# Optimization experiments

Measured on AMD Instinct MI355X. Metric: run time of the kernel, lower is better.

The kernel has to match this reference:

```python
import jax, jax.numpy as jnp
import numpy as np

B, T, M, P = 512, 64, 256, 256


def setup_inputs() -> dict:
    key = jax.random.key(0)
    ks = jax.random.split(key, 17)
    w = lambda i, shape: (jax.random.normal(ks[i], shape, jnp.float32) * 0.05)
    return {
        "encoded_inputs": jax.random.normal(ks[0], (B, T, M), jnp.float32),
        "y": jax.random.normal(ks[1], (B, T, 1), jnp.float32),
        "tar": jax.random.normal(ks[2], (B, 2), jnp.float32),
        "train": 1,
        "Wd_w": w(3, (M, 2 * P)), "Wd_b": w(4, (M,)),
        "Ud_w": w(5, (M, M)),
        "vd_w": w(6, (1, M)),
        "wt_w": w(7, (1, M + 1)), "wt_b": w(8, (1,)),
        "Wy_w": w(9, (P, P + M)), "Wy_b": w(10, (P,)),
        "vy_w": w(11, (1, P)), "vy_b": w(12, (1,)),
        "Wih": w(13, (4 * P, 1)), "Whh": w(14, (4 * P, P)),
        "bih": w(15, (4 * P,)), "bhh": w(16, (4 * P,)),
    }


def _lstm_cell(x, h, c, Wih, Whh, bih, bhh):
    # torch.nn.LSTMCell gate order: i, f, g, o
    g = x @ Wih.T + h @ Whh.T + (bih + bhh)
    i, f, gg, o = jnp.split(g, 4, axis=1)
    c = jax.nn.sigmoid(f) * c + jax.nn.sigmoid(i) * jnp.tanh(gg)
    h = jax.nn.sigmoid(o) * jnp.tanh(c)
    return h, c


def reference(encoded_inputs, y, tar, train,
              Wd_w, Wd_b, Ud_w, vd_w, wt_w, wt_b,
              Wy_w, Wy_b, vy_w, vy_b, Wih, Whh, bih, bhh):
    Bn = encoded_inputs.shape[0]
    Pn = Whh.shape[1]
    Mn = encoded_inputs.shape[2]
    h0 = jnp.zeros((Bn, Pn), encoded_inputs.dtype)
    c0 = jnp.zeros((Bn, Pn), encoded_inputs.dtype)
    ctx0 = jnp.zeros((Bn, Mn), encoded_inputs.dtype)
    # U_d(encoded_inputs) is loop-invariant
    y1 = jnp.einsum('btm,nm->btn', encoded_inputs, Ud_w)  # (B,T,M)

    def attend(h, s):
        x1 = jnp.concatenate([h, s], axis=1) @ Wd_w.T + Wd_b      # (B,M)
        z1 = jnp.tanh(x1[:, None, :] + y1)                        # (B,T,M)
        l = jnp.einsum('btm,m->bt', z1, vd_w[0])                  # (B,T)
        beta = jax.nn.softmax(l, axis=1)
        return jnp.einsum('bt,btm->bm', beta, encoded_inputs)     # (B,M)

    def step(carry, y_t):
        h, s, _ = carry
        c_t = attend(h, s)
        y_til = jnp.concatenate([c_t, y_t], axis=1) @ wt_w.T + wt_b  # (B,1)
        h, s = _lstm_cell(y_til, h, s, Wih, Whh, bih, bhh)
        return (h, s, c_t), None

    (h, s, c_t), _ = jax.lax.scan(step, (h0, c0, ctx0), jnp.swapaxes(y, 0, 1))

    def head(h):
        return (jnp.concatenate([h, c_t], axis=1) @ Wy_w.T + Wy_b) @ vy_w.T + vy_b

    def extra(h, s, inp):
        y_til = jnp.concatenate([c_t, inp], axis=1) @ wt_w.T + wt_b
        h, s = _lstm_cell(y_til, h, s, Wih, Whh, bih, bhh)
        return h, s, head(h)

    y_Tp1 = head(h)
    if train:
        h, s, y_Tp2 = extra(h, s, tar[:, 0:1])
        h, s, y_Tp3 = extra(h, s, tar[:, 1:2])
    else:
        h, s, y_Tp2 = extra(h, s, y_Tp1)
        h, s, y_Tp3 = extra(h, s, y_Tp2)
    return (y_Tp1, y_Tp2, y_Tp3)
```

## Files before the change

### kernel.cpp

```cpp
#include <hip/hip_runtime.h>


typedef unsigned short u16;
typedef unsigned int u32;
typedef _Float16 half_t;
typedef half_t h2 __attribute__((ext_vector_type(2)));

#define BB 512
#define TT 64
#define MM 256
#define YS 264
#define ES 68
#define NROW 2
#define NTH 1024

#define WD16_OFF  0
#define WHH16_OFF 131072
#define WY16_OFF  393216
#define WQ_ELEMS  524288
#define WQ_BYTES  (WQ_ELEMS * 2)

struct H8 { h2 p[4]; };

#if defined(__has_builtin)
#if __has_builtin(__builtin_amdgcn_fdot2)
#define FDOT2(a, b, c) __builtin_amdgcn_fdot2((a), (b), (c), false)
#endif
#endif
#ifndef FDOT2
__device__ __forceinline__ float FDOT2(h2 a, h2 b, float c) {
  return c + (float)a[0] * (float)b[0] + (float)a[1] * (float)b[1];
}
#endif

__device__ __forceinline__ float dot8(const H8 w, const H8 a, float acc) {
  acc = FDOT2(w.p[0], a.p[0], acc);
  acc = FDOT2(w.p[1], a.p[1], acc);
  acc = FDOT2(w.p[2], a.p[2], acc);
  acc = FDOT2(w.p[3], a.p[3], acc);
  return acc;
}
__device__ __forceinline__ u16 f2h(float f) {
  union { half_t h; u16 u; } x; x.h = (half_t)f; return x.u;
}
__device__ __forceinline__ float h2f(u16 u) {
  union { u16 u; half_t h; } x; x.u = u; return (float)x.h;
}
__device__ __forceinline__ u32 pack2h(float a, float b) {
  union { h2 h; u32 u; } x;
  x.h[0] = (half_t)a; x.h[1] = (half_t)b;
  return x.u;
}
__device__ __forceinline__ h2 u2h2(u32 u) {
  union { u32 u; h2 h; } x; x.u = u; return x.h;
}
__device__ __forceinline__ void unpackH8(const H8 v, float f[8]) {
#pragma unroll
  for (int i = 0; i < 8; ++i) f[i] = (float)v.p[i >> 1][i & 1];
}
__device__ __forceinline__ void ldf8(const float* p, float f[8]) {
  float4 a = *(const float4*)p;
  float4 b = *(const float4*)(p + 4);
  f[0]=a.x; f[1]=a.y; f[2]=a.z; f[3]=a.w;
  f[4]=b.x; f[5]=b.y; f[6]=b.z; f[7]=b.w;
}
__device__ __forceinline__ float tanh_fast(float x) {
  float e = __builtin_amdgcn_exp2f(x * 2.885390081777927f);
  return 1.0f - 2.0f * __builtin_amdgcn_rcpf(1.0f + e);
}
__device__ __forceinline__ float sigmoid_fast(float x) {
  float e = __builtin_amdgcn_exp2f(x * -1.4426950408889634f);
  return __builtin_amdgcn_rcpf(1.0f + e);
}

__global__ __launch_bounds__(256) void prep_kernel(
    const float* __restrict__ Wd, const float* __restrict__ Whh,
    const float* __restrict__ Wy, u16* __restrict__ o) {
  int i = blockIdx.x * 256 + threadIdx.x;
  float v;
  if (i < WHH16_OFF) {
    int ki = i & 7, n = (i >> 3) & 255, kb = i >> 11;
    v = Wd[n * 512 + kb * 8 + ki];
  } else if (i < WY16_OFF) {
    int r = i - WHH16_OFF;
    int ki = r & 7, n = (r >> 3) & 1023, kb = r >> 13;
    v = Whh[n * 256 + kb * 8 + ki];
  } else {
    int r = i - WY16_OFF;
    int ki = r & 7, n = (r >> 3) & 255, kb = r >> 11;
    v = Wy[n * 512 + kb * 8 + ki];
  }
  o[i] = f2h(v);
}

template <int WQ>
__global__ __launch_bounds__(NTH, 4) void scan_kernel(
    const float* __restrict__ E,
    const float* __restrict__ yin,
    const float* __restrict__ tar,
    const int*   __restrict__ train,
    const void*  __restrict__ Wd_q,
    const float* __restrict__ Wd_b,
    const float* __restrict__ Ud_w,
    const float* __restrict__ vd_w,
    const float* __restrict__ wt_w,
    const float* __restrict__ wt_b,
    const void*  __restrict__ Wy_q,
    const float* __restrict__ Wy_b,
    const float* __restrict__ vy_w,
    const float* __restrict__ vy_b,
    const float* __restrict__ Wih,
    const void*  __restrict__ Whh_q,
    const float* __restrict__ bih,
    const float* __restrict__ bhh,
    float* __restrict__ out)
{
  __shared__ __align__(16) u16   y1l[NROW][TT * YS];
  __shared__ __align__(16) u16   e16T[NROW][MM * ES];
  __shared__ __align__(16) u32   hs16[NROW][256];
  __shared__ __align__(16) u32   ctx16p[NROW][128];
  __shared__ __align__(16) float px1[8][MM];
  __shared__ __align__(16) u32   pgs32[8][MM];
  __shared__ __align__(16) float lpart[NROW][4][TT];
  __shared__ __align__(16) u16   betas16[8][TT];
  __shared__ __align__(16) float ysh[NROW][TT];
  __shared__ __align__(16) float ewl[NROW][TT];
  __shared__ float red[16];
  __shared__ float sc[NROW];

  const int j   = threadIdx.x;
  const int n   = j & 255;
  const int grp = j >> 8;
  const int wv  = j >> 6;
  const int b0  = blockIdx.x * NROW;

  if (j < 512) ((u32*)hs16)[j] = 0;
  float creg0 = 0.f, creg1 = 0.f;

  const float wih0 = Wih[n],       wih1 = Wih[n + 256];
  const float wih2 = Wih[n + 512], wih3 = Wih[n + 768];
  const float bb0 = bih[n]       + bhh[n];
  const float bb1 = bih[n + 256] + bhh[n + 256];
  const float bb2 = bih[n + 512] + bhh[n + 512];
  const float bb3 = bih[n + 768] + bhh[n + 768];
  const float wtM = wt_w[MM], wtb = wt_b[0];

  if (j < NROW * TT) {
    const int r = j >> 6, t = j & 63;
    ysh[r][t] = yin[(size_t)(b0 + r) * TT + t];
    const float* __restrict__ Er = E + ((size_t)(b0 + r) * TT + t) * MM;
    float acc = 0.f;
    for (int m0 = 0; m0 < MM; m0 += 8) {
      float e[8], w[8];
      ldf8(Er + m0, e); ldf8(wt_w + m0, w);
#pragma unroll
      for (int m = 0; m < 8; ++m) acc = fmaf(e[m], w[m], acc);
    }
    ewl[r][t] = acc;
  }

  {
    const float* __restrict__ Eb0 = E + (size_t)b0 * TT * MM;
    for (int i = j; i < NROW * TT * MM; i += NTH) {
      int r = i >> 14;
      int idx = i & 16383;
      int t = idx >> 8, m = idx & 255;
      e16T[r][m * ES + t] = f2h(Eb0[i]);
    }
  }

  {
    const int rs = grp >> 1, ths = grp & 1;
    const float* __restrict__ Eb = E + (size_t)(b0 + rs) * TT * MM;
    const float* __restrict__ Uj = Ud_w + (size_t)n * MM;
    for (int t0 = ths * 32; t0 < ths * 32 + 32; t0 += 16) {
      float acc[16];
#pragma unroll
      for (int i = 0; i < 16; ++i) acc[i] = 0.f;
      for (int m0 = 0; m0 < MM; m0 += 8) {
        float w[8]; ldf8(Uj + m0, w);
#pragma unroll
        for (int tt = 0; tt < 16; ++tt) {
          float e[8]; ldf8(Eb + (size_t)(t0 + tt) * MM + m0, e);
#pragma unroll
          for (int mm = 0; mm < 8; ++mm) acc[tt] = fmaf(e[mm], w[mm], acc[tt]);
        }
      }
#pragma unroll
      for (int tt = 0; tt < 16; ++tt)
        y1l[rs][(t0 + tt) * YS + n] = f2h(acc[tt]);
    }
  }
  __syncthreads();

  auto gates_apply = [&](int r, float gi, float gf, float gg, float go,
                         float ytil) {
    gi += ytil * wih0 + bb0;
    gf += ytil * wih1 + bb1;
    gg += ytil * wih2 + bb2;
    go += ytil * wih3 + bb3;
    float& cr = r ? creg1 : creg0;
    float c = sigmoid_fast(gf) * cr + sigmoid_fast(gi) * tanh_fast(gg);
    float h = sigmoid_fast(go) * tanh_fast(c);
    cr = c;
    u16* hsu = (u16*)hs16[r];
    hsu[n] = f2h(h);
    hsu[256 + n] = f2h(c);
  };

  auto whh_gates = [&]() {
    if (wv >= 8) {
      const int jj = j - 512;
      const int n2 = jj & 255, half = jj >> 8;
      float a00 = 0, a01 = 0, a10 = 0, a11 = 0;
      float a20 = 0, a21 = 0, a30 = 0, a31 = 0;
      if (WQ) {
        const u16* __restrict__ base =
            (const u16*)Whh_q + ((size_t)(half * 16) * 1024 + n2) * 8;
#pragma unroll 2
        for (int i = 0; i < 16; ++i) {
          const u16* p = base + (size_t)i * 8192;
          H8 w0 = *(const H8*)p;
          H8 w1 = *(const H8*)(p + 2048);
          H8 w2 = *(const H8*)(p + 4096);
          H8 w3 = *(const H8*)(p + 6144);
          const int kb = half * 16 + i;
          H8 h0v = *(const H8*)&hs16[0][kb * 4];
          H8 h1v = *(const H8*)&hs16[1][kb * 4];
          a00 = dot8(w0, h0v, a00); a01 = dot8(w0, h1v, a01);
          a10 = dot8(w1, h0v, a10); a11 = dot8(w1, h1v, a11);
          a20 = dot8(w2, h0v, a20); a21 = dot8(w2, h1v, a21);
          a30 = dot8(w3, h0v, a30); a31 = dot8(w3, h1v, a31);
        }
      } else {
        const float* __restrict__ base =
            (const float*)Whh_q + (size_t)n2 * 256 + half * 128;
#pragma unroll 2
        for (int i = 0; i < 16; ++i) {
          const int kb = half * 16 + i;
          H8 h0v = *(const H8*)&hs16[0][kb * 4];
          H8 h1v = *(const H8*)&hs16[1][kb * 4];
          float hf0[8], hf1[8]; unpackH8(h0v, hf0); unpackH8(h1v, hf1);
          float w0[8], w1[8], w2[8], w3[8];
          ldf8(base + i * 8, w0);
          ldf8(base + 256 * 256 + i * 8, w1);
          ldf8(base + 512 * 256 + i * 8, w2);
          ldf8(base + 768 * 256 + i * 8, w3);
#pragma unroll
          for (int m = 0; m < 8; ++m) {
            a00 = fmaf(hf0[m], w0[m], a00); a01 = fmaf(hf1[m], w0[m], a01);
            a10 = fmaf(hf0[m], w1[m], a10); a11 = fmaf(hf1[m], w1[m], a11);
            a20 = fmaf(hf0[m], w2[m], a20); a21 = fmaf(hf1[m], w2[m], a21);
            a30 = fmaf(hf0[m], w3[m], a30); a31 = fmaf(hf1[m], w3[m], a31);
          }
        }
      }
      pgs32[(0 << 1) | half][n2] = pack2h(a00, a01);
      pgs32[(1 << 1) | half][n2] = pack2h(a10, a11);
      pgs32[(2 << 1) | half][n2] = pack2h(a20, a21);
      pgs32[(3 << 1) | half][n2] = pack2h(a30, a31);
    }
  };

  auto gates_combine_apply = [&](float yt0, float yt1) {
    h2 i0 = u2h2(pgs32[0][n]), i1 = u2h2(pgs32[1][n]);
    h2 f0 = u2h2(pgs32[2][n]), f1 = u2h2(pgs32[3][n]);
    h2 g0 = u2h2(pgs32[4][n]), g1 = u2h2(pgs32[5][n]);
    h2 o0 = u2h2(pgs32[6][n]), o1 = u2h2(pgs32[7][n]);
    gates_apply(0, (float)i0[0] + (float)i1[0], (float)f0[0] + (float)f1[0],
                (float)g0[0] + (float)g1[0], (float)o0[0] + (float)o1[0], yt0);
    gates_apply(1, (float)i0[1] + (float)i1[1], (float)f0[1] + (float)f1[1],
                (float)g0[1] + (float)g1[1], (float)o0[1] + (float)o1[1], yt1);
  };

  auto head_store = [&](int outIdx) {
    float p = 0.f;
    const int rr = grp >> 1, seg = grp & 1;
    const u32* st = seg ? ctx16p[rr] : hs16[rr];
    if (WQ) {
      const u16* pw = (const u16*)Wy_q + ((size_t)(seg * 32) * 256 + n) * 8;
#pragma unroll 2
      for (int kb = 0; kb < 32; ++kb) {
        H8 w = *(const H8*)pw; pw += 2048;
        H8 s = *(const H8*)&st[kb * 4];
        p = dot8(w, s, p);
      }
    } else {
      const float* W = (const float*)Wy_q + (size_t)n * 512 + seg * 256;
#pragma unroll 2
      for (int kb = 0; kb < 32; ++kb) {
        H8 sv = *(const H8*)&st[kb * 4];
        float sf[8]; unpackH8(sv, sf);
        float w[8]; ldf8(W + kb * 8, w);
#pragma unroll
        for (int i = 0; i < 8; ++i) p = fmaf(sf[i], w[i], p);
      }
    }
    if (grp) px1[grp - 1][n] = p;
    __syncthreads();
    if (grp == 0) {
      float q0 = (p + px1[0][n] + Wy_b[n]) * vy_w[n];
      float q1 = (px1[1][n] + px1[2][n] + Wy_b[n]) * vy_w[n];
#pragma unroll
      for (int off = 32; off; off >>= 1) {
        q0 += __shfl_xor(q0, off, 64);
        q1 += __shfl_xor(q1, off, 64);
      }
      if ((j & 63) == 0) { red[wv] = q0; red[4 + wv] = q1; }
    }
    __syncthreads();
    if (j == 0) {
      float o0 = red[0] + red[1] + red[2] + red[3] + vy_b[0];
      float o1 = red[4] + red[5] + red[6] + red[7] + vy_b[0];
      out[(size_t)outIdx * BB + b0] = o0;
      out[(size_t)outIdx * BB + b0 + 1] = o1;
      sc[0] = o0; sc[1] = o1;
    }
    __syncthreads();
  };

  for (int step = 0; step < TT; ++step) {
    {
      float ax0 = 0.f, ax1 = 0.f;
      if (WQ) {
        const u16* pd = (const u16*)Wd_q + ((size_t)(grp * 16) * 256 + n) * 8;
#pragma unroll 4
        for (int i = 0; i < 16; ++i) {
          H8 w = *(const H8*)pd; pd += 2048;
          const int kb = grp * 16 + i;
          H8 s0 = *(const H8*)&hs16[0][kb * 4];
          H8 s1 = *(const H8*)&hs16[1][kb * 4];
          ax0 = dot8(w, s0, ax0);
          ax1 = dot8(w, s1, ax1);
        }
      } else {
        const float* pd = (const float*)Wd_q + (size_t)n * 512 + grp * 128;
#pragma unroll 2
        for (int i = 0; i < 16; ++i) {
          const int kb = grp * 16 + i;
          H8 s0v = *(const H8*)&hs16[0][kb * 4];
          H8 s1v = *(const H8*)&hs16[1][kb * 4];
          float f0[8], f1[8]; unpackH8(s0v, f0); unpackH8(s1v, f1);
          float w[8]; ldf8(pd + i * 8, w);
#pragma unroll
          for (int m = 0; m < 8; ++m) {
            ax0 = fmaf(f0[m], w[m], ax0);
            ax1 = fmaf(f1[m], w[m], ax1);
          }
        }
      }
      if (grp == 0) { float b = Wd_b[n]; ax0 += b; ax1 += b; }
      px1[grp][n] = ax0;
      px1[4 + grp][n] = ax1;
    }
    __syncthreads();

    if (wv < 8) {
      const int r = j >> 8, e4 = (j >> 6) & 3, t = j & 63;
      const int mb = e4 * 64;
      const u16* __restrict__ yrow = &y1l[r][t * YS + mb];
      const float* __restrict__ p0 = &px1[(r << 2) | 0][mb];
      const float* __restrict__ p1 = &px1[(r << 2) | 1][mb];
      const float* __restrict__ p2 = &px1[(r << 2) | 2][mb];
      const float* __restrict__ p3 = &px1[(r << 2) | 3][mb];
      const float* __restrict__ vp = vd_w + mb;
      float lp = 0.f;
#pragma unroll 2
      for (int m0 = 0; m0 < 64; m0 += 8) {
        float xa[8], xb[8], xc[8], xd[8], vf[8], yf[8];
        ldf8(p0 + m0, xa); ldf8(p1 + m0, xb);
        ldf8(p2 + m0, xc); ldf8(p3 + m0, xd);
        H8 yv = *(const H8*)(yrow + m0); unpackH8(yv, yf);
        ldf8(vp + m0, vf);
#pragma unroll
        for (int mm = 0; mm < 8; ++mm) {
          float z = tanh_fast(xa[mm] + xb[mm] + xc[mm] + xd[mm] + yf[mm]);
          lp = fmaf(z, vf[mm], lp);
        }
      }
      lpart[r][e4][t] = lp;
    } else {
      whh_gates();
    }
    __syncthreads();

    if (j < 256) {
      const int t = j & 63;
      float l0 = lpart[0][0][t] + lpart[0][1][t] + lpart[0][2][t] +
                 lpart[0][3][t];
      float l1 = lpart[1][0][t] + lpart[1][1][t] + lpart[1][2][t] +
                 lpart[1][3][t];
      float m0v = l0, m1v = l1;
#pragma unroll
      for (int off = 32; off; off >>= 1) {
        m0v = fmaxf(m0v, __shfl_xor(m0v, off, 64));
        m1v = fmaxf(m1v, __shfl_xor(m1v, off, 64));
      }
      float e0 = __builtin_amdgcn_exp2f((l0 - m0v) * 1.4426950408889634f);
      float e1 = __builtin_amdgcn_exp2f((l1 - m1v) * 1.4426950408889634f);
      float se0 = e0, sy0 = e0 * ewl[0][t];
      float se1 = e1, sy1 = e1 * ewl[1][t];
#pragma unroll
      for (int off = 32; off; off >>= 1) {
        se0 += __shfl_xor(se0, off, 64); sy0 += __shfl_xor(sy0, off, 64);
        se1 += __shfl_xor(se1, off, 64); sy1 += __shfl_xor(sy1, off, 64);
      }
      float yt0 = sy0 * __builtin_amdgcn_rcpf(se0) + ysh[0][step] * wtM + wtb;
      float yt1 = sy1 * __builtin_amdgcn_rcpf(se1) + ysh[1][step] * wtM + wtb;
      gates_combine_apply(yt0, yt1);
    }
    __syncthreads();
  }

  if (j < 512) {
    const int r = j >> 8, lane = j & 63;
    float l = lpart[r][0][lane] + lpart[r][1][lane] + lpart[r][2][lane] +
              lpart[r][3][lane];
    float mx = l;
#pragma unroll
    for (int off = 32; off; off >>= 1) mx = fmaxf(mx, __shfl_xor(mx, off, 64));
    float e = __builtin_amdgcn_exp2f((l - mx) * 1.4426950408889634f);
    float sm = e;
#pragma unroll
    for (int off = 32; off; off >>= 1) sm += __shfl_xor(sm, off, 64);
    betas16[wv][lane] = f2h(e * __builtin_amdgcn_rcpf(sm));
    asm volatile("s_waitcnt lgkmcnt(0)" ::: "memory");
    const u16* __restrict__ bp = betas16[wv];
    const u16* __restrict__ ep = &e16T[r][n * ES];
    float acc = 0.f;
#pragma unroll
    for (int t0 = 0; t0 < TT; t0 += 8) {
      H8 bv = *(const H8*)(bp + t0);
      h2 e0 = *(const h2*)(ep + t0);
      h2 e1 = *(const h2*)(ep + t0 + 2);
      h2 e2 = *(const h2*)(ep + t0 + 4);
      h2 e3 = *(const h2*)(ep + t0 + 6);
      acc = FDOT2(bv.p[0], e0, acc);
      acc = FDOT2(bv.p[1], e1, acc);
      acc = FDOT2(bv.p[2], e2, acc);
      acc = FDOT2(bv.p[3], e3, acc);
    }
    ((u16*)ctx16p[r])[n] = f2h(acc);
  }
  __syncthreads();

  if (j < 512) {
    const int r = j >> 8;
    float p = h2f(((const u16*)ctx16p[r])[n]) * wt_w[n];
#pragma unroll
    for (int off = 32; off; off >>= 1) p += __shfl_xor(p, off, 64);
    if ((j & 63) == 0) red[wv] = p;
  }
  __syncthreads();
  const float ctd0 = red[0] + red[1] + red[2] + red[3];
  const float ctd1 = red[4] + red[5] + red[6] + red[7];

  head_store(0);

  const int tr = train[0];
  for (int e = 0; e < 2; ++e) {
    whh_gates();
    __syncthreads();
    if (j < 256) {
      float inp0 = tr ? tar[(size_t)b0 * 2 + e] : sc[0];
      float inp1 = tr ? tar[(size_t)(b0 + 1) * 2 + e] : sc[1];
      float yt0 = ctd0 + inp0 * wtM + wtb;
      float yt1 = ctd1 + inp1 * wtM + wtb;
      gates_combine_apply(yt0, yt1);
    }
    __syncthreads();
    head_store(1 + e);
  }
}

extern "C" void kernel_launch(void* const* d_in, const int* in_sizes, int n_in,
                              void* d_out, int out_size, void* d_ws, size_t ws_size,
                              hipStream_t stream) {
  const float* E     = (const float*)d_in[0];
  const float* yin   = (const float*)d_in[1];
  const float* tar   = (const float*)d_in[2];
  const int*   train = (const int*)d_in[3];
  const float* Wd_w  = (const float*)d_in[4];
  const float* Wd_b  = (const float*)d_in[5];
  const float* Ud_w  = (const float*)d_in[6];
  const float* vd_w  = (const float*)d_in[7];
  const float* wt_w  = (const float*)d_in[8];
  const float* wt_b  = (const float*)d_in[9];
  const float* Wy_w  = (const float*)d_in[10];
  const float* Wy_b  = (const float*)d_in[11];
  const float* vy_w  = (const float*)d_in[12];
  const float* vy_b  = (const float*)d_in[13];
  const float* Wih   = (const float*)d_in[14];
  const float* Whh   = (const float*)d_in[15];
  const float* bih   = (const float*)d_in[16];
  const float* bhh   = (const float*)d_in[17];

  float* out = (float*)d_out;

  if (ws_size >= (size_t)WQ_BYTES) {
    u16* wq = (u16*)d_ws;
    prep_kernel<<<dim3(WQ_ELEMS / 256), dim3(256), 0, stream>>>(
        Wd_w, Whh, Wy_w, wq);
    scan_kernel<1><<<dim3(BB / NROW), dim3(NTH), 0, stream>>>(
        E, yin, tar, train, wq + WD16_OFF, Wd_b, Ud_w, vd_w, wt_w, wt_b,
        wq + WY16_OFF, Wy_b, vy_w, vy_b, Wih, wq + WHH16_OFF, bih, bhh, out);
  } else {
    scan_kernel<0><<<dim3(BB / NROW), dim3(NTH), 0, stream>>>(
        E, yin, tar, train, Wd_w, Wd_b, Ud_w, vd_w, wt_w, wt_b,
        Wy_w, Wy_b, vy_w, vy_b, Wih, Whh, bih, bhh, out);
  }

  (void)in_sizes; (void)n_in; (void)out_size;
}
```

Baseline: 1.046 ms.

## Cache part of Whh in LDS and compute final context from global E

Drops the per-block fp16 transposed copy of the encoder inputs from shared memory. The final context vector is now computed once, directly from fp32 global E, after the softmax betas are stored in fp32. The freed LDS holds the first quarter of the fp16 Whh weights, so part of the recurrent gate matvec reads LDS instead of global/L2 each step. It also moves the second row's head reduction to separate red slots, avoiding overlap with the wv 4-7 entries written by the ctx reduction. The risks are a startup copy cost and a branch inside the fully unrolled gate loop.

```diff
diff --git a/kernel.cpp b/kernel.cpp
--- a/kernel.cpp
+++ b/kernel.cpp
@@ -10,7 +10,6 @@
 #define TT 64
 #define MM 256
 #define YS 264
-#define ES 68
 #define NROW 2
 #define NTH 1024
 
@@ -42,9 +41,6 @@
 }
 __device__ __forceinline__ u16 f2h(float f) {
   union { half_t h; u16 u; } x; x.h = (half_t)f; return x.u;
-}
-__device__ __forceinline__ float h2f(u16 u) {
-  union { u16 u; half_t h; } x; x.u = u; return (float)x.h;
 }
 __device__ __forceinline__ u32 pack2h(float a, float b) {
   union { h2 h; u32 u; } x;
@@ -116,13 +112,13 @@
     float* __restrict__ out)
 {
   __shared__ __align__(16) u16   y1l[NROW][TT * YS];
-  __shared__ __align__(16) u16   e16T[NROW][MM * ES];
+  __shared__ __align__(16) u16   whhc[4 * 1024 * 8];
   __shared__ __align__(16) u32   hs16[NROW][256];
   __shared__ __align__(16) u32   ctx16p[NROW][128];
   __shared__ __align__(16) float px1[8][MM];
   __shared__ __align__(16) u32   pgs32[8][MM];
   __shared__ __align__(16) float lpart[NROW][4][TT];
-  __shared__ __align__(16) u16   betas16[8][TT];
+  __shared__ __align__(16) float bet[NROW][TT];
   __shared__ __align__(16) float ysh[NROW][TT];
   __shared__ __align__(16) float ewl[NROW][TT];
   __shared__ float red[16];
@@ -144,6 +140,12 @@
   const float bb2 = bih[n + 512] + bhh[n + 512];
   const float bb3 = bih[n + 768] + bhh[n + 768];
   const float wtM = wt_w[MM], wtb = wt_b[0];
+
+  if (WQ) {
+    const u32* __restrict__ src = (const u32*)Whh_q;
+    u32* __restrict__ dst = (u32*)whhc;
+    for (int i = j; i < 16384; i += NTH) dst[i] = src[i];
+  }
 
   if (j < NROW * TT) {
     const int r = j >> 6, t = j & 63;
@@ -157,16 +159,6 @@
       for (int m = 0; m < 8; ++m) acc = fmaf(e[m], w[m], acc);
     }
     ewl[r][t] = acc;
-  }
-
-  {
-    const float* __restrict__ Eb0 = E + (size_t)b0 * TT * MM;
-    for (int i = j; i < NROW * TT * MM; i += NTH) {
-      int r = i >> 14;
-      int idx = i & 16383;
-      int t = idx >> 8, m = idx & 255;
-      e16T[r][m * ES + t] = f2h(Eb0[i]);
-    }
   }
 
   {
@@ -217,13 +209,22 @@
       if (WQ) {
         const u16* __restrict__ base =
             (const u16*)Whh_q + ((size_t)(half * 16) * 1024 + n2) * 8;
-#pragma unroll 2
+#pragma unroll
         for (int i = 0; i < 16; ++i) {
-          const u16* p = base + (size_t)i * 8192;
-          H8 w0 = *(const H8*)p;
-          H8 w1 = *(const H8*)(p + 2048);
-          H8 w2 = *(const H8*)(p + 4096);
-          H8 w3 = *(const H8*)(p + 6144);
+          H8 w0, w1, w2, w3;
+          if (i < 4 && half == 0) {
+            const u16* p = whhc + ((size_t)i * 1024 + n2) * 8;
+            w0 = *(const H8*)p;
+            w1 = *(const H8*)(p + 2048);
+            w2 = *(const H8*)(p + 4096);
+            w3 = *(const H8*)(p + 6144);
+          } else {
+            const u16* p = base + (size_t)i * 8192;
+            w0 = *(const H8*)p;
+            w1 = *(const H8*)(p + 2048);
+            w2 = *(const H8*)(p + 4096);
+            w3 = *(const H8*)(p + 6144);
+          }
           const int kb = half * 16 + i;
           H8 h0v = *(const H8*)&hs16[0][kb * 4];
           H8 h1v = *(const H8*)&hs16[1][kb * 4];
@@ -306,12 +307,12 @@
         q0 += __shfl_xor(q0, off, 64);
         q1 += __shfl_xor(q1, off, 64);
       }
-      if ((j & 63) == 0) { red[wv] = q0; red[4 + wv] = q1; }
+      if ((j & 63) == 0) { red[wv] = q0; red[8 + wv] = q1; }
     }
     __syncthreads();
     if (j == 0) {
       float o0 = red[0] + red[1] + red[2] + red[3] + vy_b[0];
-      float o1 = red[4] + red[5] + red[6] + red[7] + vy_b[0];
+      float o1 = red[8] + red[9] + red[10] + red[11] + vy_b[0];
       out[(size_t)outIdx * BB + b0] = o0;
       out[(size_t)outIdx * BB + b0 + 1] = o1;
       sc[0] = o0; sc[1] = o1;
@@ -412,10 +413,10 @@
     __syncthreads();
   }
 
-  if (j < 512) {
-    const int r = j >> 8, lane = j & 63;
-    float l = lpart[r][0][lane] + lpart[r][1][lane] + lpart[r][2][lane] +
-              lpart[r][3][lane];
+  if (j < NROW * TT) {
+    const int r = j >> 6, t = j & 63;
+    float l = lpart[r][0][t] + lpart[r][1][t] + lpart[r][2][t] +
+              lpart[r][3][t];
     float mx = l;
 #pragma unroll
     for (int off = 32; off; off >>= 1) mx = fmaxf(mx, __shfl_xor(mx, off, 64));
@@ -423,30 +424,19 @@
     float sm = e;
 #pragma unroll
     for (int off = 32; off; off >>= 1) sm += __shfl_xor(sm, off, 64);
-    betas16[wv][lane] = f2h(e * __builtin_amdgcn_rcpf(sm));
-    asm volatile("s_waitcnt lgkmcnt(0)" ::: "memory");
-    const u16* __restrict__ bp = betas16[wv];
-    const u16* __restrict__ ep = &e16T[r][n * ES];
-    float acc = 0.f;
-#pragma unroll
-    for (int t0 = 0; t0 < TT; t0 += 8) {
-      H8 bv = *(const H8*)(bp + t0);
-      h2 e0 = *(const h2*)(ep + t0);
-      h2 e1 = *(const h2*)(ep + t0 + 2);
-      h2 e2 = *(const h2*)(ep + t0 + 4);
-      h2 e3 = *(const h2*)(ep + t0 + 6);
-      acc = FDOT2(bv.p[0], e0, acc);
-      acc = FDOT2(bv.p[1], e1, acc);
-      acc = FDOT2(bv.p[2], e2, acc);
-      acc = FDOT2(bv.p[3], e3, acc);
-    }
-    ((u16*)ctx16p[r])[n] = f2h(acc);
+    bet[r][t] = e * __builtin_amdgcn_rcpf(sm);
   }
   __syncthreads();
 
   if (j < 512) {
     const int r = j >> 8;
-    float p = h2f(((const u16*)ctx16p[r])[n]) * wt_w[n];
+    const float* __restrict__ Eb = E + (size_t)(b0 + r) * TT * MM + n;
+    float acc = 0.f;
+#pragma unroll 8
+    for (int t = 0; t < TT; ++t)
+      acc = fmaf(bet[r][t], Eb[(size_t)t * MM], acc);
+    ((u16*)ctx16p[r])[n] = f2h(acc);
+    float p = acc * wt_w[n];
 #pragma unroll
     for (int off = 32; off; off >>= 1) p += __shfl_xor(p, off, 64);
     if ((j & 63) == 0) red[wv] = p;
```

Result: slower. 2.465 ms (+135.5%).
